# Performance work log

Hardware: AMD Instinct MI355X
Metric: run time of the kernel (lower is better)

Reference implementation:

```python
import jax, jax.numpy as jnp
import numpy as np

C = 128      # block channels
K = 7        # involution kernel size
GC = 16      # group_ch
G = (C // 2) // GC  # involution groups = 4


def conv1x1(x, w, b):
    # x: (B,Cin,H,W), w: (Cout,Cin)
    return jnp.einsum('bchw,oc->bohw', x, w) + b[None, :, None, None]


def conv2d(x, w, b, pad):
    y = jax.lax.conv_general_dilated(
        x, w, window_strides=(1, 1), padding=((pad, pad), (pad, pad)),
        dimension_numbers=('NCHW', 'OIHW', 'NCHW'))
    return y + b[None, :, None, None]


def prelu(x, a):
    return jnp.where(x >= 0, x, a * x)


def patches7(x):
    # x: (B,C,H,W) -> (B,C,K*K,H,W), same padding (torch Unfold, pad=3)
    B, Cc, H, W = x.shape
    p = K // 2
    xp = jnp.pad(x, ((0, 0), (0, 0), (p, p), (p, p)))
    return jnp.stack([xp[:, :, i:i + H, j:j + W]
                      for i in range(K) for j in range(K)], axis=2)


def setup_inputs() -> dict:
    key = jax.random.key(0)
    ks = jax.random.split(key, 9)
    f32 = jnp.float32
    def w(k, shape, s=0.02):
        return jax.random.normal(k, shape, f32) * s
    d = {}
    d['x'] = jax.random.normal(ks[0], (2, C, 128, 128), f32)
    # conv1: C -> C//2, 1x1
    d['w1'] = w(ks[1], (C // 2, C)); d['b1'] = jnp.zeros((C // 2,), f32)
    d['a1'] = jnp.float32(0.25)  # PReLU (single param)
    # involution reduce: C//2 -> C//4, 1x1 (+ReLU)
    d['wr'] = w(ks[2], (C // 4, C // 2)); d['br'] = jnp.zeros((C // 4,), f32)
    # involution span: C//4 -> G*K*K, 1x1
    d['ws'] = w(ks[3], (G * K * K, C // 4)); d['bs'] = jnp.zeros((G * K * K,), f32)
    d['a2'] = jnp.float32(0.25)
    # conv2: C//2 -> C, 1x1
    d['w2'] = w(ks[4], (C, C // 2)); d['b2'] = jnp.zeros((C,), f32)
    # attn conv: 2 -> 1, 7x7 pad 3
    d['wa'] = w(ks[5], (1, 2, 7, 7)); d['ba'] = jnp.zeros((1,), f32)
    # psec: 3x3 (C//4->C//4) + PReLU + 1x1 (C//4->C)
    d['wp1'] = w(ks[6], (C // 4, C // 4, 3, 3)); d['bp1'] = jnp.zeros((C // 4,), f32)
    d['ap'] = jnp.float32(0.25)
    d['wp2'] = w(ks[7], (C, C // 4)); d['bp2'] = jnp.zeros((C,), f32)
    return d


def reference(x, w1, b1, a1, wr, br, ws, bs, a2, w2, b2, wa, ba, wp1, bp1, ap, wp2, bp2):
    B, _, H, W = x.shape
    x1 = prelu(conv1x1(x, w1, b1), a1)                       # (B, C/2, H, W)
    # involution: per-pixel dynamic kernels
    f = jax.nn.relu(conv1x1(x1, wr, br))                     # (B, C/4, H, W)
    kw = conv1x1(f, ws, bs).reshape(B, G, 1, K * K, H, W)    # dynamic kernels
    pat = patches7(x1).reshape(B, G, GC, K * K, H, W)        # unfolded patches
    x2 = (kw * pat).sum(axis=3).reshape(B, C // 2, H, W)     # multiply-reduce
    x3 = conv1x1(prelu(x2, a2), w2, b2)                      # (B, C, H, W)
    # attention gate on f (ZPool -> 7x7 conv -> sigmoid)
    zp = jnp.concatenate([f.max(axis=1, keepdims=True),
                          f.mean(axis=1, keepdims=True)], axis=1)
    attn = jax.nn.sigmoid(conv2d(zp, wa, ba, 3))             # (B, 1, H, W)
    x4 = x3 * attn
    ps = conv1x1(prelu(conv2d(f, wp1, bp1, 1), ap), wp2, bp2)
    return x4 + ps
```

## Files before the change

kernel.cpp:

```cpp
#include <hip/hip_runtime.h>

#define HW_  16384
#define NPX  32768

__device__ __forceinline__ float prelu_(float x, float a) { return x >= 0.f ? x : a * x; }

__global__ __launch_bounds__(256, 3) void k_front(const float* __restrict__ x,
        const float* __restrict__ w1, const float* __restrict__ b1,
        const float* __restrict__ a1p, const float* __restrict__ wr,
        const float* __restrict__ br, float* __restrict__ x1,
        float* __restrict__ f, float* __restrict__ zp) {
    __shared__ float sA[12544];
    float* xs  = sA;
    float* wT1 = sA + 4096;
    int p0 = blockIdx.x << 6;
    int b = p0 >> 14, hw0 = p0 & 16383;

    for (int e = threadIdx.x; e < 8192; e += 256) {
        int o = e >> 7, c = e & 127;
        wT1[o * 132 + c] = w1[e];
    }
    int pq = threadIdx.x & 15;
    int og = threadIdx.x >> 4;
    const float a1 = a1p[0];
    float4 acc[4];
    #pragma unroll
    for (int u = 0; u < 4; ++u) { float bv = b1[og * 4 + u]; acc[u] = make_float4(bv, bv, bv, bv); }
    const float* xb = x + (b << 21) + hw0;
    #pragma unroll 1
    for (int half = 0; half < 2; ++half) {
        float4 xv[4];
        #pragma unroll
        for (int i = 0; i < 4; ++i) {
            int e = threadIdx.x + (i << 8);
            xv[i] = *(const float4*)&xb[((half * 64 + (e >> 4)) << 14) + ((e & 15) << 2)];
        }
        __syncthreads();
        #pragma unroll
        for (int i = 0; i < 4; ++i) {
            int e = threadIdx.x + (i << 8);
            *(float4*)&xs[((e >> 4) << 6) + ((e & 15) << 2)] = xv[i];
        }
        __syncthreads();
        #pragma unroll 4
        for (int c4 = 0; c4 < 16; ++c4) {
            float4 taps[4];
            #pragma unroll
            for (int j = 0; j < 4; ++j)
                taps[j] = *(const float4*)&xs[((c4 * 4 + j) << 6) + (pq << 2)];
            #pragma unroll
            for (int u = 0; u < 4; ++u) {
                float4 wv = *(const float4*)&wT1[(og * 4 + u) * 132 + half * 64 + c4 * 4];
                acc[u].x = fmaf(wv.x, taps[0].x, acc[u].x); acc[u].y = fmaf(wv.x, taps[0].y, acc[u].y);
                acc[u].z = fmaf(wv.x, taps[0].z, acc[u].z); acc[u].w = fmaf(wv.x, taps[0].w, acc[u].w);
                acc[u].x = fmaf(wv.y, taps[1].x, acc[u].x); acc[u].y = fmaf(wv.y, taps[1].y, acc[u].y);
                acc[u].z = fmaf(wv.y, taps[1].z, acc[u].z); acc[u].w = fmaf(wv.y, taps[1].w, acc[u].w);
                acc[u].x = fmaf(wv.z, taps[2].x, acc[u].x); acc[u].y = fmaf(wv.z, taps[2].y, acc[u].y);
                acc[u].z = fmaf(wv.z, taps[2].z, acc[u].z); acc[u].w = fmaf(wv.z, taps[2].w, acc[u].w);
                acc[u].x = fmaf(wv.w, taps[3].x, acc[u].x); acc[u].y = fmaf(wv.w, taps[3].y, acc[u].y);
                acc[u].z = fmaf(wv.w, taps[3].z, acc[u].z); acc[u].w = fmaf(wv.w, taps[3].w, acc[u].w);
            }
        }
    }
    float4 res[4];
    #pragma unroll
    for (int u = 0; u < 4; ++u) {
        res[u].x = prelu_(acc[u].x, a1); res[u].y = prelu_(acc[u].y, a1);
        res[u].z = prelu_(acc[u].z, a1); res[u].w = prelu_(acc[u].w, a1);
        *(float4*)(x1 + ((b * 64 + og * 4 + u) << 14) + hw0 + (pq << 2)) = res[u];
    }
    __syncthreads();
    float* x1t = sA;
    float* wrT = sA + 4352;
    float* ft  = sA + 6432;
    #pragma unroll
    for (int u = 0; u < 4; ++u)
        *(float4*)&x1t[(og * 4 + u) * 68 + (pq << 2)] = res[u];
    for (int e = threadIdx.x; e < 2048; e += 256) {
        int fo = e >> 6, c = e & 63;
        wrT[fo * 65 + c] = wr[e];
    }
    __syncthreads();
    int pq2 = threadIdx.x & 15;
    int fg = threadIdx.x >> 4;
    float4 fa[2];
    #pragma unroll
    for (int u = 0; u < 2; ++u) { float bv = br[fg * 2 + u]; fa[u] = make_float4(bv, bv, bv, bv); }
    #pragma unroll 4
    for (int c = 0; c < 64; ++c) {
        float4 tap = *(const float4*)&x1t[c * 68 + (pq2 << 2)];
        #pragma unroll
        for (int u = 0; u < 2; ++u) {
            float wv = wrT[(fg * 2 + u) * 65 + c];
            fa[u].x = fmaf(wv, tap.x, fa[u].x);
            fa[u].y = fmaf(wv, tap.y, fa[u].y);
            fa[u].z = fmaf(wv, tap.z, fa[u].z);
            fa[u].w = fmaf(wv, tap.w, fa[u].w);
        }
    }
    #pragma unroll
    for (int u = 0; u < 2; ++u) {
        float4 r;
        r.x = fmaxf(fa[u].x, 0.f); r.y = fmaxf(fa[u].y, 0.f);
        r.z = fmaxf(fa[u].z, 0.f); r.w = fmaxf(fa[u].w, 0.f);
        *(float4*)(f + ((b * 32 + fg * 2 + u) << 14) + hw0 + (pq2 << 2)) = r;
        *(float4*)&ft[(fg * 2 + u) * 68 + (pq2 << 2)] = r;
    }
    __syncthreads();
    if (threadIdx.x < 64) {
        int px = threadIdx.x;
        float mx = ft[px], sm = ft[px];
        #pragma unroll
        for (int c = 1; c < 32; ++c) {
            float v = ft[c * 68 + px];
            mx = fmaxf(mx, v); sm += v;
        }
        zp[((b * 2 + 0) << 14) + hw0 + px] = mx;
        zp[((b * 2 + 1) << 14) + hw0 + px] = sm * (1.f / 32.f);
    }
}

__global__ __launch_bounds__(256, 4) void k_mid2(const float* __restrict__ x1,
        const float* __restrict__ f, const float* __restrict__ ws_,
        const float* __restrict__ bs, float* __restrict__ x2,
        const float* __restrict__ zp, const float* __restrict__ wp1,
        const float* __restrict__ bp1, const float* __restrict__ app,
        float* __restrict__ p1, const float* __restrict__ wa,
        const float* __restrict__ ba, float* __restrict__ attn,
        const float* __restrict__ a2p) {
    __shared__ float smem[8448];
    if (blockIdx.x < 512) {
        float* tile = smem;
        int g = blockIdx.x >> 7;
        int t = blockIdx.x & 127;
        int b = t >> 6;
        int th = (t >> 3) & 7, tw = t & 7;
        int h0 = th * 16, w0 = tw * 16;
        const float* x1g = x1 + ((b * 64 + g * 16) << 14);
        #pragma unroll 1
        for (int rem = threadIdx.x; rem < 484; rem += 256) {
            int r = rem / 22, cl = rem - r * 22;
            int hh = h0 + r - 3, ww = w0 + cl - 3;
            bool ok = (hh >= 0 && hh < 128 && ww >= 0 && ww < 128);
            const float* src = x1g + (hh << 7) + ww;
            float v[16];
            #pragma unroll
            for (int c = 0; c < 16; ++c) v[c] = ok ? src[c << 14] : 0.f;
            float* dst = tile + r * 24 + cl;
            #pragma unroll
            for (int c = 0; c < 16; ++c) dst[c * 528] = v[c];
        }
        int lh = threadIdx.x >> 4, lw = threadIdx.x & 15;
        int hw = ((h0 + lh) << 7) + w0 + lw;
        float fv[32];
        const float* fp = f + (b << 19) + hw;
        #pragma unroll
        for (int c = 0; c < 32; ++c) fv[c] = fp[c << 14];
        __syncthreads();
        float acc[16];
        #pragma unroll
        for (int u = 0; u < 16; ++u) acc[u] = 0.f;
        const float* tap0 = tile + lh * 24 + lw;
        const float* wk = ws_ + g * 49 * 32;
        const float* bsg = bs + g * 49;
        #pragma unroll 1
        for (int di = 0; di < 7; ++di) {
            #pragma unroll 1
            for (int dj = 0; dj < 7; ++dj) {
                int kk = di * 7 + dj;
                float kwv = bsg[kk];
                const float* wkk = wk + kk * 32;
                #pragma unroll
                for (int c = 0; c < 32; ++c) kwv = fmaf(wkk[c], fv[c], kwv);
                const float* tp = tap0 + di * 24 + dj;
                #pragma unroll
                for (int u = 0; u < 16; ++u)
                    acc[u] = fmaf(kwv, tp[u * 528], acc[u]);
            }
        }
        const float a2 = a2p[0];
        float* op = x2 + ((b * 64 + g * 16) << 14) + hw;
        #pragma unroll
        for (int u = 0; u < 16; ++u) op[u << 14] = prelu_(acc[u], a2);
    } else if (blockIdx.x < 1024) {
        float* fs = smem;
        float* wT = smem + 6080;
        int bid = blockIdx.x - 512;
        int half = bid >> 8;
        int t = bid & 255;
        int b = t >> 7;
        int tl = t & 127;
        int th = tl >> 3, tw = tl & 7;
        int h0 = th * 8, w0 = tw * 16;
        int o0 = half * 16;
        const float* fb = f + (b << 19);
        #pragma unroll 1
        for (int rem = threadIdx.x; rem < 180; rem += 256) {
            int r = rem / 18, cl = rem - r * 18;
            int hh = h0 + r - 1, ww = w0 + cl - 1;
            bool ok = (hh >= 0 && hh < 128 && ww >= 0 && ww < 128);
            const float* src = fb + (hh << 7) + ww;
            float* dst = fs + r * 19 + cl;
            #pragma unroll 1
            for (int cb = 0; cb < 4; ++cb) {
                float v[8];
                #pragma unroll
                for (int c = 0; c < 8; ++c) v[c] = ok ? src[(cb * 8 + c) << 14] : 0.f;
                #pragma unroll
                for (int c = 0; c < 8; ++c) dst[(cb * 8 + c) * 190] = v[c];
            }
        }
        int pxq = threadIdx.x & 31;
        int rowq = pxq >> 2, colq = pxq & 3;
        int oh = threadIdx.x >> 5;
        const float ap = app[0];
        float acc[2][4];
        #pragma unroll
        for (int o = 0; o < 2; ++o) {
            float bv = bp1[o0 + oh * 2 + o];
            #pragma unroll
            for (int px = 0; px < 4; ++px) acc[o][px] = bv;
        }
        const float* fsb = fs + rowq * 19 + colq * 4;
        #pragma unroll 1
        for (int cih = 0; cih < 2; ++cih) {
            __syncthreads();
            #pragma unroll 1
            for (int e = threadIdx.x; e < 2304; e += 256) {
                int o = e / 144, i = e - o * 144;
                wT[o * 145 + i] = wp1[(o0 + o) * 288 + cih * 144 + i];
            }
            __syncthreads();
            #pragma unroll 1
            for (int cl_ = 0; cl_ < 16; ++cl_) {
                int ci = cih * 16 + cl_;
                float tap[3][6];
                const float* base = fsb + ci * 190;
                #pragma unroll
                for (int r = 0; r < 3; ++r)
                    #pragma unroll
                    for (int j = 0; j < 6; ++j)
                        tap[r][j] = base[r * 19 + j];
                #pragma unroll
                for (int ki = 0; ki < 3; ++ki)
                    #pragma unroll
                    for (int kj = 0; kj < 3; ++kj) {
                        int idx = cl_ * 9 + ki * 3 + kj;
                        float w0v = wT[(oh * 2 + 0) * 145 + idx];
                        float w1v = wT[(oh * 2 + 1) * 145 + idx];
                        #pragma unroll
                        for (int px = 0; px < 4; ++px) {
                            float tv = tap[ki][px + kj];
                            acc[0][px] = fmaf(w0v, tv, acc[0][px]);
                            acc[1][px] = fmaf(w1v, tv, acc[1][px]);
                        }
                    }
            }
        }
        int hw = ((h0 + rowq) << 7) + w0 + colq * 4;
        #pragma unroll
        for (int o = 0; o < 2; ++o) {
            float4 r;
            r.x = prelu_(acc[o][0], ap); r.y = prelu_(acc[o][1], ap);
            r.z = prelu_(acc[o][2], ap); r.w = prelu_(acc[o][3], ap);
            *(float4*)(p1 + ((b * 32 + o0 + oh * 2 + o) << 14) + hw) = r;
        }
    } else {
        float* zs = smem;
        int t = blockIdx.x - 1024;
        int b = t >> 6;
        int tile = t & 63;
        int th = tile >> 3, tw = tile & 7;
        int h0 = th * 16, w0 = tw * 16;
        const float* zb = zp + (b << 15);
        #pragma unroll 1
        for (int rem = threadIdx.x; rem < 484; rem += 256) {
            int r = rem / 22, cl = rem - r * 22;
            int hh = h0 + r - 3, ww = w0 + cl - 3;
            bool ok = (hh >= 0 && hh < 128 && ww >= 0 && ww < 128);
            const float* src = zb + (hh << 7) + ww;
            float v0 = ok ? src[0] : 0.f;
            float v1 = ok ? src[HW_] : 0.f;
            zs[r * 23 + cl] = v0;
            zs[506 + r * 23 + cl] = v1;
        }
        __syncthreads();
        int lh = threadIdx.x >> 4, lw = threadIdx.x & 15;
        float acc = ba[0];
        #pragma unroll
        for (int c = 0; c < 2; ++c) {
            const float* zc = &zs[c * 506 + lh * 23 + lw];
            #pragma unroll
            for (int i = 0; i < 7; ++i)
                #pragma unroll
                for (int j = 0; j < 7; ++j)
                    acc = fmaf(wa[c * 49 + i * 7 + j], zc[i * 23 + j], acc);
        }
        attn[(b << 14) + ((h0 + lh) << 7) + w0 + lw] = 1.f / (1.f + expf(-acc));
    }
}

__global__ __launch_bounds__(256, 4) void k_final(const float* __restrict__ x2p,
        const float* __restrict__ p1, const float* __restrict__ attn,
        const float* __restrict__ w2, const float* __restrict__ b2,
        const float* __restrict__ wp2, const float* __restrict__ bp2,
        float* __restrict__ out) {
    __shared__ float wT2[64 * 20];
    __shared__ float wTp[32 * 20];
    int split = blockIdx.x >> 7;
    int tile = blockIdx.x & 127;
    int p0 = tile << 8;
    int b = p0 >> 14, hw0 = p0 & 16383;
    int o0 = split * 16;

    for (int e = threadIdx.x; e < 1024; e += 256) {
        int o = e & 15, c = e >> 4;
        wT2[c * 20 + o] = w2[(o0 + o) * 64 + c];
    }
    for (int e = threadIdx.x; e < 512; e += 256) {
        int o = e & 15, c = e >> 4;
        wTp[c * 20 + o] = wp2[(o0 + o) * 32 + c];
    }
    int q4 = threadIdx.x & 63;
    int og = threadIdx.x >> 6;
    float b2v[4], bpv[4];
    #pragma unroll
    for (int u = 0; u < 4; ++u) { b2v[u] = b2[o0 + og * 4 + u]; bpv[u] = bp2[o0 + og * 4 + u]; }
    float4 acc[4];
    #pragma unroll
    for (int u = 0; u < 4; ++u) acc[u] = make_float4(0.f, 0.f, 0.f, 0.f);
    __syncthreads();

    const float* xb = x2p + (b << 20) + hw0 + (q4 << 2);
    #pragma unroll 1
    for (int cb = 0; cb < 8; ++cb) {
        float4 xv[8];
        #pragma unroll
        for (int j = 0; j < 8; ++j) xv[j] = *(const float4*)&xb[(cb * 8 + j) << 14];
        #pragma unroll
        for (int j = 0; j < 8; ++j) {
            float4 wv = *(const float4*)&wT2[(cb * 8 + j) * 20 + og * 4];
            acc[0].x = fmaf(wv.x, xv[j].x, acc[0].x); acc[0].y = fmaf(wv.x, xv[j].y, acc[0].y);
            acc[0].z = fmaf(wv.x, xv[j].z, acc[0].z); acc[0].w = fmaf(wv.x, xv[j].w, acc[0].w);
            acc[1].x = fmaf(wv.y, xv[j].x, acc[1].x); acc[1].y = fmaf(wv.y, xv[j].y, acc[1].y);
            acc[1].z = fmaf(wv.y, xv[j].z, acc[1].z); acc[1].w = fmaf(wv.y, xv[j].w, acc[1].w);
            acc[2].x = fmaf(wv.z, xv[j].x, acc[2].x); acc[2].y = fmaf(wv.z, xv[j].y, acc[2].y);
            acc[2].z = fmaf(wv.z, xv[j].z, acc[2].z); acc[2].w = fmaf(wv.z, xv[j].w, acc[2].w);
            acc[3].x = fmaf(wv.w, xv[j].x, acc[3].x); acc[3].y = fmaf(wv.w, xv[j].y, acc[3].y);
            acc[3].z = fmaf(wv.w, xv[j].z, acc[3].z); acc[3].w = fmaf(wv.w, xv[j].w, acc[3].w);
        }
    }
    float4 at = *(const float4*)(attn + (b << 14) + hw0 + (q4 << 2));
    #pragma unroll
    for (int u = 0; u < 4; ++u) {
        acc[u].x = (acc[u].x + b2v[u]) * at.x + bpv[u];
        acc[u].y = (acc[u].y + b2v[u]) * at.y + bpv[u];
        acc[u].z = (acc[u].z + b2v[u]) * at.z + bpv[u];
        acc[u].w = (acc[u].w + b2v[u]) * at.w + bpv[u];
    }
    const float* pb = p1 + (b << 19) + hw0 + (q4 << 2);
    #pragma unroll 1
    for (int cb = 0; cb < 4; ++cb) {
        float4 pv[8];
        #pragma unroll
        for (int j = 0; j < 8; ++j) pv[j] = *(const float4*)&pb[(cb * 8 + j) << 14];
        #pragma unroll
        for (int j = 0; j < 8; ++j) {
            float4 wv = *(const float4*)&wTp[(cb * 8 + j) * 20 + og * 4];
            acc[0].x = fmaf(wv.x, pv[j].x, acc[0].x); acc[0].y = fmaf(wv.x, pv[j].y, acc[0].y);
            acc[0].z = fmaf(wv.x, pv[j].z, acc[0].z); acc[0].w = fmaf(wv.x, pv[j].w, acc[0].w);
            acc[1].x = fmaf(wv.y, pv[j].x, acc[1].x); acc[1].y = fmaf(wv.y, pv[j].y, acc[1].y);
            acc[1].z = fmaf(wv.y, pv[j].z, acc[1].z); acc[1].w = fmaf(wv.y, pv[j].w, acc[1].w);
            acc[2].x = fmaf(wv.z, pv[j].x, acc[2].x); acc[2].y = fmaf(wv.z, pv[j].y, acc[2].y);
            acc[2].z = fmaf(wv.z, pv[j].z, acc[2].z); acc[2].w = fmaf(wv.z, pv[j].w, acc[2].w);
            acc[3].x = fmaf(wv.w, pv[j].x, acc[3].x); acc[3].y = fmaf(wv.w, pv[j].y, acc[3].y);
            acc[3].z = fmaf(wv.w, pv[j].z, acc[3].z); acc[3].w = fmaf(wv.w, pv[j].w, acc[3].w);
        }
    }
    #pragma unroll
    for (int u = 0; u < 4; ++u)
        *(float4*)(out + ((b * 128 + o0 + og * 4 + u) << 14) + hw0 + (q4 << 2)) = acc[u];
}

extern "C" void kernel_launch(void* const* d_in, const int* in_sizes, int n_in,
                              void* d_out, int out_size, void* d_ws, size_t ws_size,
                              hipStream_t stream) {
    const float* x   = (const float*)d_in[0];
    const float* w1  = (const float*)d_in[1];
    const float* b1  = (const float*)d_in[2];
    const float* a1  = (const float*)d_in[3];
    const float* wr  = (const float*)d_in[4];
    const float* br  = (const float*)d_in[5];
    const float* ws_ = (const float*)d_in[6];
    const float* bs  = (const float*)d_in[7];
    const float* a2  = (const float*)d_in[8];
    const float* w2  = (const float*)d_in[9];
    const float* b2  = (const float*)d_in[10];
    const float* wa  = (const float*)d_in[11];
    const float* ba  = (const float*)d_in[12];
    const float* wp1 = (const float*)d_in[13];
    const float* bp1 = (const float*)d_in[14];
    const float* ap  = (const float*)d_in[15];
    const float* wp2 = (const float*)d_in[16];
    const float* bp2 = (const float*)d_in[17];
    float* out = (float*)d_out;

    float* w = (float*)d_ws;
    float* ws_x1   = w;
    float* ws_f    = ws_x1 + 2 * 64 * HW_;
    float* ws_x2   = ws_f  + 2 * 32 * HW_;
    float* ws_zp   = ws_x2 + 2 * 64 * HW_;
    float* ws_attn = ws_zp + 2 * 2 * HW_;
    float* ws_p1   = ws_attn + NPX;

    hipLaunchKernelGGL(k_front, dim3(512), dim3(256), 0, stream,
                       x, w1, b1, a1, wr, br, ws_x1, ws_f, ws_zp);
    hipLaunchKernelGGL(k_mid2, dim3(1152), dim3(256), 0, stream,
                       ws_x1, ws_f, ws_, bs, ws_x2, ws_zp,
                       wp1, bp1, ap, ws_p1, wa, ba, ws_attn, a2);
    hipLaunchKernelGGL(k_final, dim3(1024), dim3(256), 0, stream,
                       ws_x2, ws_p1, ws_attn, w2, b2, wp2, bp2, out);
}
```

Baseline: 174.5 us.

## Compute two pixels per thread in involution, chunk channels, vectorize 3x3 conv loads

The involution branch now has each thread handle two adjacent pixels, so each dynamic-kernel weight read is shared across both pixels. Its x1 halo tile is staged in two 8-channel chunks to bound shared memory, which halves the involution block count. The 3x3 conv branch pads its shared layouts so it can use float4/float2 loads for taps and weights instead of scalar LDS. The price is higher register pressure (launch bounds lowered to 3) and fewer blocks for the involution work.

```diff
diff --git a/kernel.cpp b/kernel.cpp
--- a/kernel.cpp
+++ b/kernel.cpp
@@ -120,7 +120,7 @@
     }
 }
 
-__global__ __launch_bounds__(256, 4) void k_mid2(const float* __restrict__ x1,
+__global__ __launch_bounds__(256, 3) void k_mid2(const float* __restrict__ x1,
         const float* __restrict__ f, const float* __restrict__ ws_,
         const float* __restrict__ bs, float* __restrict__ x2,
         const float* __restrict__ zp, const float* __restrict__ wp1,
@@ -128,64 +128,83 @@
         float* __restrict__ p1, const float* __restrict__ wa,
         const float* __restrict__ ba, float* __restrict__ attn,
         const float* __restrict__ a2p) {
-    __shared__ float smem[8448];
-    if (blockIdx.x < 512) {
+    __shared__ float smem[9472];
+    if (blockIdx.x < 256) {
         float* tile = smem;
-        int g = blockIdx.x >> 7;
-        int t = blockIdx.x & 127;
-        int b = t >> 6;
-        int th = (t >> 3) & 7, tw = t & 7;
-        int h0 = th * 16, w0 = tw * 16;
+        int g = blockIdx.x >> 6;
+        int t = blockIdx.x & 63;
+        int b = t >> 5;
+        int tl = t & 31;
+        int th = tl >> 2, tw = tl & 3;
+        int h0 = th * 16, w0 = tw * 32;
+        int lh = threadIdx.x >> 4;
+        int pc = threadIdx.x & 15;
+        int hw = ((h0 + lh) << 7) + w0 + pc * 2;
+        const float* fp = f + (b << 19) + hw;
+        float2 fv[32];
+        #pragma unroll
+        for (int c = 0; c < 32; ++c) fv[c] = *(const float2*)&fp[c << 14];
+        float2 acc[16];
+        #pragma unroll
+        for (int u = 0; u < 16; ++u) acc[u] = make_float2(0.f, 0.f);
         const float* x1g = x1 + ((b * 64 + g * 16) << 14);
-        #pragma unroll 1
-        for (int rem = threadIdx.x; rem < 484; rem += 256) {
-            int r = rem / 22, cl = rem - r * 22;
-            int hh = h0 + r - 3, ww = w0 + cl - 3;
-            bool ok = (hh >= 0 && hh < 128 && ww >= 0 && ww < 128);
-            const float* src = x1g + (hh << 7) + ww;
-            float v[16];
-            #pragma unroll
-            for (int c = 0; c < 16; ++c) v[c] = ok ? src[c << 14] : 0.f;
-            float* dst = tile + r * 24 + cl;
-            #pragma unroll
-            for (int c = 0; c < 16; ++c) dst[c * 528] = v[c];
-        }
-        int lh = threadIdx.x >> 4, lw = threadIdx.x & 15;
-        int hw = ((h0 + lh) << 7) + w0 + lw;
-        float fv[32];
-        const float* fp = f + (b << 19) + hw;
-        #pragma unroll
-        for (int c = 0; c < 32; ++c) fv[c] = fp[c << 14];
-        __syncthreads();
-        float acc[16];
-        #pragma unroll
-        for (int u = 0; u < 16; ++u) acc[u] = 0.f;
-        const float* tap0 = tile + lh * 24 + lw;
         const float* wk = ws_ + g * 49 * 32;
         const float* bsg = bs + g * 49;
         #pragma unroll 1
-        for (int di = 0; di < 7; ++di) {
+        for (int ch = 0; ch < 2; ++ch) {
+            __syncthreads();
             #pragma unroll 1
-            for (int dj = 0; dj < 7; ++dj) {
-                int kk = di * 7 + dj;
-                float kwv = bsg[kk];
-                const float* wkk = wk + kk * 32;
-                #pragma unroll
-                for (int c = 0; c < 32; ++c) kwv = fmaf(wkk[c], fv[c], kwv);
-                const float* tp = tap0 + di * 24 + dj;
-                #pragma unroll
-                for (int u = 0; u < 16; ++u)
-                    acc[u] = fmaf(kwv, tp[u * 528], acc[u]);
+            for (int rem = threadIdx.x; rem < 836; rem += 256) {
+                int r = rem / 38, cl = rem - r * 38;
+                int hh = h0 + r - 3, ww = w0 + cl - 3;
+                bool ok = (hh >= 0 && hh < 128 && ww >= 0 && ww < 128);
+                const float* src = x1g + ((ch * 8) << 14) + (hh << 7) + ww;
+                float v[8];
+                #pragma unroll
+                for (int c = 0; c < 8; ++c) v[c] = ok ? src[c << 14] : 0.f;
+                float* dst = tile + r * 40 + cl;
+                #pragma unroll
+                for (int c = 0; c < 8; ++c) dst[c * 880] = v[c];
+            }
+            __syncthreads();
+            const float* tap0 = tile + lh * 40 + pc * 2;
+            #pragma unroll 1
+            for (int di = 0; di < 7; ++di) {
+                #pragma unroll 1
+                for (int dj = 0; dj < 7; ++dj) {
+                    int kk = di * 7 + dj;
+                    float bsv = bsg[kk];
+                    float2 kwv = make_float2(bsv, bsv);
+                    const float* wkk = wk + kk * 32;
+                    #pragma unroll
+                    for (int c = 0; c < 32; ++c) {
+                        float wc = wkk[c];
+                        kwv.x = fmaf(wc, fv[c].x, kwv.x);
+                        kwv.y = fmaf(wc, fv[c].y, kwv.y);
+                    }
+                    const float* tp = tap0 + di * 40 + dj;
+                    #pragma unroll
+                    for (int u = 0; u < 8; ++u) {
+                        float t0 = tp[u * 880];
+                        float t1 = tp[u * 880 + 1];
+                        acc[ch * 8 + u].x = fmaf(kwv.x, t0, acc[ch * 8 + u].x);
+                        acc[ch * 8 + u].y = fmaf(kwv.y, t1, acc[ch * 8 + u].y);
+                    }
+                }
             }
         }
         const float a2 = a2p[0];
         float* op = x2 + ((b * 64 + g * 16) << 14) + hw;
         #pragma unroll
-        for (int u = 0; u < 16; ++u) op[u << 14] = prelu_(acc[u], a2);
-    } else if (blockIdx.x < 1024) {
+        for (int u = 0; u < 16; ++u) {
+            float2 r;
+            r.x = prelu_(acc[u].x, a2); r.y = prelu_(acc[u].y, a2);
+            *(float2*)&op[u << 14] = r;
+        }
+    } else if (blockIdx.x < 768) {
         float* fs = smem;
-        float* wT = smem + 6080;
-        int bid = blockIdx.x - 512;
+        float* wT = smem + 6400;
+        int bid = blockIdx.x - 256;
         int half = bid >> 8;
         int t = bid & 255;
         int b = t >> 7;
@@ -200,14 +219,14 @@
             int hh = h0 + r - 1, ww = w0 + cl - 1;
             bool ok = (hh >= 0 && hh < 128 && ww >= 0 && ww < 128);
             const float* src = fb + (hh << 7) + ww;
-            float* dst = fs + r * 19 + cl;
+            float* dst = fs + r * 20 + cl;
             #pragma unroll 1
             for (int cb = 0; cb < 4; ++cb) {
                 float v[8];
                 #pragma unroll
                 for (int c = 0; c < 8; ++c) v[c] = ok ? src[(cb * 8 + c) << 14] : 0.f;
                 #pragma unroll
-                for (int c = 0; c < 8; ++c) dst[(cb * 8 + c) * 190] = v[c];
+                for (int c = 0; c < 8; ++c) dst[(cb * 8 + c) * 200] = v[c];
             }
         }
         int pxq = threadIdx.x & 31;
@@ -221,38 +240,49 @@
             #pragma unroll
             for (int px = 0; px < 4; ++px) acc[o][px] = bv;
         }
-        const float* fsb = fs + rowq * 19 + colq * 4;
+        const float* fsb = fs + rowq * 20 + colq * 4;
         #pragma unroll 1
         for (int cih = 0; cih < 2; ++cih) {
             __syncthreads();
             #pragma unroll 1
             for (int e = threadIdx.x; e < 2304; e += 256) {
-                int o = e / 144, i = e - o * 144;
-                wT[o * 145 + i] = wp1[(o0 + o) * 288 + cih * 144 + i];
+                int o = e / 144, rem = e - o * 144;
+                int cl_ = rem / 9, k = rem - cl_ * 9;
+                wT[o * 192 + cl_ * 12 + k] = wp1[(o0 + o) * 288 + cih * 144 + rem];
             }
             __syncthreads();
             #pragma unroll 1
             for (int cl_ = 0; cl_ < 16; ++cl_) {
                 int ci = cih * 16 + cl_;
+                const float* base = fsb + ci * 200;
                 float tap[3][6];
-                const float* base = fsb + ci * 190;
-                #pragma unroll
-                for (int r = 0; r < 3; ++r)
-                    #pragma unroll
-                    for (int j = 0; j < 6; ++j)
-                        tap[r][j] = base[r * 19 + j];
+                #pragma unroll
+                for (int r = 0; r < 3; ++r) {
+                    float4 t4 = *(const float4*)&base[r * 20];
+                    float2 t2 = *(const float2*)&base[r * 20 + 4];
+                    tap[r][0] = t4.x; tap[r][1] = t4.y; tap[r][2] = t4.z;
+                    tap[r][3] = t4.w; tap[r][4] = t2.x; tap[r][5] = t2.y;
+                }
+                const float* wb0 = &wT[(oh * 2 + 0) * 192 + cl_ * 12];
+                const float* wb1 = &wT[(oh * 2 + 1) * 192 + cl_ * 12];
+                float4 wa0 = *(const float4*)wb0;
+                float4 wa1 = *(const float4*)(wb0 + 4);
+                float  wa2 = wb0[8];
+                float4 wc0 = *(const float4*)wb1;
+                float4 wc1 = *(const float4*)(wb1 + 4);
+                float  wc2 = wb1[8];
+                float w0a[9] = {wa0.x, wa0.y, wa0.z, wa0.w, wa1.x, wa1.y, wa1.z, wa1.w, wa2};
+                float w1a[9] = {wc0.x, wc0.y, wc0.z, wc0.w, wc1.x, wc1.y, wc1.z, wc1.w, wc2};
                 #pragma unroll
                 for (int ki = 0; ki < 3; ++ki)
                     #pragma unroll
                     for (int kj = 0; kj < 3; ++kj) {
-                        int idx = cl_ * 9 + ki * 3 + kj;
-                        float w0v = wT[(oh * 2 + 0) * 145 + idx];
-                        float w1v = wT[(oh * 2 + 1) * 145 + idx];
+                        int k = ki * 3 + kj;
                         #pragma unroll
                         for (int px = 0; px < 4; ++px) {
                             float tv = tap[ki][px + kj];
-                            acc[0][px] = fmaf(w0v, tv, acc[0][px]);
-                            acc[1][px] = fmaf(w1v, tv, acc[1][px]);
+                            acc[0][px] = fmaf(w0a[k], tv, acc[0][px]);
+                            acc[1][px] = fmaf(w1a[k], tv, acc[1][px]);
                         }
                     }
             }
@@ -267,7 +297,7 @@
         }
     } else {
         float* zs = smem;
-        int t = blockIdx.x - 1024;
+        int t = blockIdx.x - 768;
         int b = t >> 6;
         int tile = t & 63;
         int th = tile >> 3, tw = tile & 7;
@@ -415,7 +445,7 @@
 
     hipLaunchKernelGGL(k_front, dim3(512), dim3(256), 0, stream,
                        x, w1, b1, a1, wr, br, ws_x1, ws_f, ws_zp);
-    hipLaunchKernelGGL(k_mid2, dim3(1152), dim3(256), 0, stream,
+    hipLaunchKernelGGL(k_mid2, dim3(896), dim3(256), 0, stream,
                        ws_x1, ws_f, ws_, bs, ws_x2, ws_zp,
                        wp1, bp1, ap, ws_p1, wa, ba, ws_attn, a2);
     hipLaunchKernelGGL(k_final, dim3(1024), dim3(256), 0, stream,
```

New measurement: 185.0 us. 1.06x slower.
